# Optimization experiments

Hardware: AMD Instinct MI355X
Metric: run time of the kernel (lower is better)

## Reference

```python
import jax, jax.numpy as jnp
import numpy as np

H = 512   # hidden_state_sizes
E = 512   # embedding_size
L = 2     # num_rnn_layers
VGG = 4096


def gru_cell(x, h, Wu, bu, Wr, br, Wc, bc):
    # stacked = cat(x, h) along features; rows of W: first input, then hidden
    s = jnp.concatenate([x, h], axis=1)
    r = jax.nn.sigmoid(s @ Wr + br)
    u = jax.nn.sigmoid(s @ Wu + bu)
    s1 = jnp.concatenate([x, r * h], axis=1)
    c = jnp.tanh(s1 @ Wc + bc)
    return u * h + (1.0 - u) * c


def setup_inputs() -> dict:
    key = jax.random.key(0)
    ks = jax.random.split(key, 10)
    B, T, V = 128, 40, 10000
    N = E + H  # concat width (layer0: E+H == H+H since E==H)
    sc = float(np.sqrt(1.0 / N))
    return dict(
        xTokens=jax.random.randint(ks[0], (B, T), 0, V),
        vgg_fc7=jax.random.normal(ks[1], (B, VGG), jnp.float32),
        embedding=jax.random.normal(ks[2], (V, E), jnp.float32) * 0.02,
        W_in=jax.random.normal(ks[3], (VGG, H), jnp.float32) * float(np.sqrt(1.0 / VGG)),
        b_in=jnp.zeros((H,), jnp.float32),
        W_u=jax.random.normal(ks[4], (L, N, H), jnp.float32) * sc,
        b_u=jnp.zeros((L, H), jnp.float32),
        W_r=jax.random.normal(ks[5], (L, N, H), jnp.float32) * sc,
        b_r=jnp.zeros((L, H), jnp.float32),
        W_c=jax.random.normal(ks[6], (L, N, H), jnp.float32) * sc,
        b_c=jnp.zeros((L, H), jnp.float32),
        W_out=jax.random.normal(ks[7], (H, V), jnp.float32) * float(np.sqrt(1.0 / H)),
        b_out=jnp.zeros((V,), jnp.float32),
    )


def reference(xTokens, vgg_fc7, embedding, W_in, b_in, W_u, b_u, W_r, b_r,
              W_c, b_c, W_out, b_out):
    # initial hidden state from image features, shared across rnn layers
    h0 = jnp.tanh(vgg_fc7 @ W_in + b_in)                # [B,H]
    h = jnp.broadcast_to(h0, (L,) + h0.shape)           # [L,B,H]
    x = embedding[xTokens]                              # [B,T,E]
    xs = jnp.swapaxes(x, 0, 1)                          # [T,B,E] (scan over time)

    def step(h, xt):
        hs = []
        inp = xt
        for j in range(L):  # small fixed layer loop
            hj = gru_cell(inp, h[j], W_u[j], b_u[j], W_r[j], b_r[j], W_c[j], b_c[j])
            hs.append(hj)
            inp = hj
        logit = inp @ W_out + b_out                     # [B,V]
        return jnp.stack(hs), logit

    h_final, logits = jax.lax.scan(step, h, xs)         # logits [T,B,V]
    return jnp.swapaxes(logits, 0, 1), h_final
```

## Files before the change

### kernel.cpp

```cpp
#include <hip/hip_runtime.h>
#include <hip/hip_bf16.h>
#include <math.h>

typedef __bf16 bf16_t;
typedef __bf16 bf16x8 __attribute__((ext_vector_type(8)));
typedef float  f32x4 __attribute__((ext_vector_type(4)));
typedef float  f4    __attribute__((ext_vector_type(4)));
typedef float  f2    __attribute__((ext_vector_type(2)));
typedef unsigned short u16x4 __attribute__((ext_vector_type(4)));
typedef unsigned long long u64;

#define HS  512
#define BB  128
#define TT  40
#define VV  10000
#define VGGN 4096
#define SLOT ((size_t)65536)
#define NBLK 96
#define NGRID 256

#define CL(h, idx) ((((h) * 164) + (idx)) * 64)
#define CRH0(h,s) CL(h, (s))
#define CHB0(h,s) CL(h, 41 + (s))
#define CRH1(h,s) CL(h, 82 + (s))
#define CHB1(h,s) CL(h, 123 + (s))
#define XGR(t)    ((328 + (t)) * 64)
#define NSYNCW (368 * 64)

__device__ __forceinline__ void cst64(void* p, u64 v) {
  __hip_atomic_store((u64*)p, v, __ATOMIC_RELAXED, __HIP_MEMORY_SCOPE_AGENT);
}
__device__ __forceinline__ void cst32(float* p, float v) {
  __hip_atomic_store(p, v, __ATOMIC_RELAXED, __HIP_MEMORY_SCOPE_AGENT);
}

__device__ __forceinline__ void slot_inc(unsigned* sync, int line)
{
  __syncthreads();
  asm volatile("" ::: "memory");
  if (threadIdx.x == 0)
    __hip_atomic_fetch_add(&sync[line], 1u, __ATOMIC_RELAXED,
                           __HIP_MEMORY_SCOPE_AGENT);
}

template<int SLP>
__device__ __forceinline__ void slot_wait(unsigned* sync, int line,
                                          unsigned target)
{
  if (threadIdx.x == 0) {
    while (__hip_atomic_load(&sync[line], __ATOMIC_RELAXED,
                             __HIP_MEMORY_SCOPE_AGENT) < target)
      __builtin_amdgcn_s_sleep(SLP);
  }
  asm volatile("" ::: "memory");
  __syncthreads();
}

template<int SLP>
__device__ __forceinline__ void slot_wait2(unsigned* sync, int lineA,
                                           unsigned tA, int lineB, unsigned tB)
{
  if (threadIdx.x == 0) {
    while (__hip_atomic_load(&sync[lineA], __ATOMIC_RELAXED,
                             __HIP_MEMORY_SCOPE_AGENT) < tA)
      __builtin_amdgcn_s_sleep(SLP);
    while (__hip_atomic_load(&sync[lineB], __ATOMIC_RELAXED,
                             __HIP_MEMORY_SCOPE_AGENT) < tB)
      __builtin_amdgcn_s_sleep(SLP);
  }
  asm volatile("" ::: "memory");
  __syncthreads();
}

struct MiscArgs {
  unsigned* sync;
  const float *bu, *br, *bc;
  float* xbias;
  const float* vgg; bf16_t* vggb;
  const int* tok; const float* emb; bf16_t* Aemb;
};
__global__ __launch_bounds__(256) void prep_misc(MiscArgs M)
{
  const int b = blockIdx.x, tid = threadIdx.x;
  if (b == 0) {
    for (int i = tid; i < NSYNCW; i += 256) M.sync[i] = 0u;
  } else if (b < 13) {
    int i = (b - 1) * 256 + tid;
    if (i < 2 * 1536) {
      int j = i / 1536, qq = i % 1536;
      int g = qq >> 9, n = qq & 511;
      const float* src = (g == 0) ? M.bu : (g == 1) ? M.br : M.bc;
      M.xbias[i] = src[j * 512 + n];
    }
  } else if (b < 525) {
    int i = (b - 13) * 256 + tid;
    f4 v = ((const f4*)M.vgg)[i];
    M.vggb[i * 4 + 0] = (bf16_t)v[0]; M.vggb[i * 4 + 1] = (bf16_t)v[1];
    M.vggb[i * 4 + 2] = (bf16_t)v[2]; M.vggb[i * 4 + 3] = (bf16_t)v[3];
  } else {
    int blk = b - 525;
    int m = blk * 2 + (tid >> 7);
    int t = m >> 7, bb = m & 127;
    int tk = M.tok[bb * TT + t];
    int i = tid & 127;
    f4 v = *(const f4*)(M.emb + (size_t)tk * 512 + i * 4);
    bf16_t* dst = M.Aemb + (size_t)m * 512 + i * 4;
    dst[0] = (bf16_t)v[0]; dst[1] = (bf16_t)v[1];
    dst[2] = (bf16_t)v[2]; dst[3] = (bf16_t)v[3];
  }
}

struct PArgs {
  const bf16_t *Btru0, *Bt1ru, *Btc0, *Btc1;
  const float  *bu, *br, *bc, *hs0init;
  float *xg0;
  const bf16_t *Aemb, *Btx0;
  const float  *xbias;
  bf16_t *hb0_seq, *hb1_seq, *rh0s, *rh1s;
  const bf16_t *Wto;
  const float  *bo;
  float *out, *out_hfin;
  unsigned *sync;
};

template<int K, int NF>
__device__ __forceinline__ void tile_gemm64(
    const bf16_t* __restrict__ A0, const bf16_t* __restrict__ A1,
    const bf16_t* Bs, int wave, int lane, f32x4 (&acc)[NF])
{
  const int l15 = lane & 15, kg = lane >> 4;
  const int mw = wave * 16;
#pragma unroll
  for (int f = 0; f < NF; ++f)
#pragma unroll
    for (int e = 0; e < 4; ++e) acc[f][e] = 0.f;

#pragma unroll
  for (int kk = 0; kk < K; kk += 32) {
    const bf16_t* Asrc = (kk < 512) ? A0 : A1;
    const int kc = (kk < 512 ? kk : kk - 512) + kg * 8;
    bf16x8 a = *(const bf16x8*)(Asrc + (size_t)(mw + l15) * 512 + kc);
    bf16x8 b[NF];
#pragma unroll
    for (int f = 0; f < NF; ++f) {
      int row = f * 16 + l15;
      int byteoff = row * (2 * K) + ((2 * kk + 16 * kg) ^ ((row & 7) << 4));
      b[f] = *(const bf16x8*)((const char*)Bs + byteoff);
    }
#pragma unroll
    for (int f = 0; f < NF; ++f)
      acc[f] = __builtin_amdgcn_mfma_f32_16x16x32_bf16(a, b[f], acc[f], 0, 0, 0);
  }
}

template<int C>
__device__ __forceinline__ void publish64(
    bf16_t* dst, int row0, int n0, float (&v)[2][4],
    unsigned short (*tb)[36], int wave, int lane, int tid)
{
  const int l15 = lane & 15, kg = lane >> 4;
  const int mw = wave * 16;
  constexpr int NFp = C / 16;
#pragma unroll
  for (int f = 0; f < NFp; ++f)
#pragma unroll
    for (int e = 0; e < 4; ++e)
      tb[mw + kg * 4 + e][f * 16 + l15] =
          __builtin_bit_cast(unsigned short, (bf16_t)v[f][e]);
  __syncthreads();
  constexpr int NU = 64 * C / 4;
  constexpr int IT = (NU + 255) / 256;
#pragma unroll
  for (int it = 0; it < IT; ++it) {
    int lin = it * 256 + tid;
    if (lin < NU) {
      int row = lin / (C / 4);
      int cc  = (lin % (C / 4)) * 4;
      u16x4 pk = { tb[row][cc], tb[row][cc + 1], tb[row][cc + 2], tb[row][cc + 3] };
      cst64(dst + (size_t)(row0 + row) * 512 + n0 + cc, __builtin_bit_cast(u64, pk));
    }
  }
}

__global__ __launch_bounds__(256) void gru_persist(PArgs P)
{
  const int bid = blockIdx.x, tid = threadIdx.x;
  const int wave = tid >> 6, lane = tid & 63;
  const int l15 = lane & 15, kg = lane >> 4;
  unsigned* sync = P.sync;

  __threadfence();
  __syncthreads();

  if (bid >= NBLK) {
    const int w = bid - NBLK;
    const int wm = (wave >> 1) * 64, wn = (wave & 1) * 64;

    for (int tau = w; tau < TT * 12; tau += (NGRID - NBLK)) {
      const int t = tau / 12, nb = tau % 12;
      const int bm = t * 128, bn = nb * 128;
      const bf16_t* Ap = P.Aemb + (size_t)(bm + wm + l15) * 512 + kg * 8;
      const bf16_t* Bp = P.Btx0 + (size_t)(bn + wn + l15) * 512 + kg * 8;
      f32x4 acc[4][4];
#pragma unroll
      for (int i = 0; i < 4; ++i)
#pragma unroll
        for (int j = 0; j < 4; ++j)
#pragma unroll
          for (int e = 0; e < 4; ++e) acc[i][j][e] = 0.f;
      for (int kk = 0; kk < 512; kk += 32) {
        bf16x8 a[4], b[4];
#pragma unroll
        for (int i = 0; i < 4; ++i) a[i] = *(const bf16x8*)(Ap + (size_t)i * 16 * 512 + kk);
#pragma unroll
        for (int j = 0; j < 4; ++j) b[j] = *(const bf16x8*)(Bp + (size_t)j * 16 * 512 + kk);
#pragma unroll
        for (int i = 0; i < 4; ++i)
#pragma unroll
          for (int j = 0; j < 4; ++j)
            acc[i][j] = __builtin_amdgcn_mfma_f32_16x16x32_bf16(a[i], b[j], acc[i][j], 0, 0, 0);
      }
#pragma unroll
      for (int fm = 0; fm < 4; ++fm) {
#pragma unroll
        for (int fn = 0; fn < 4; ++fn) {
          int n = bn + wn + fn * 16 + l15;
          float bv = P.xbias[n];
#pragma unroll
          for (int e = 0; e < 4; ++e) {
            int m = bm + wm + fm * 16 + kg * 4 + e;
            cst32(&P.xg0[(size_t)m * 1536 + n], acc[fm][fn][e] + bv);
          }
        }
      }
      slot_inc(sync, XGR(t));
    }

    for (int tau = w; tau < TT * 79; tau += (NGRID - NBLK)) {
      const int t = tau / 79, nb = tau % 79;
      slot_wait2<64>(sync, CHB1(0, t + 1), 32u, CHB1(1, t + 1), 32u);
      const bf16_t* A = P.hb1_seq + (size_t)(t + 1) * SLOT;
      const bf16_t* Bp = P.Wto + (size_t)(nb * 128 + wn + l15) * 512 + kg * 8;
      f32x4 acc[4][4];
#pragma unroll
      for (int i = 0; i < 4; ++i)
#pragma unroll
        for (int j = 0; j < 4; ++j)
#pragma unroll
          for (int e = 0; e < 4; ++e) acc[i][j][e] = 0.f;
      for (int kk = 0; kk < 512; kk += 32) {
        bf16x8 a[4], b[4];
#pragma unroll
        for (int i = 0; i < 4; ++i)
          a[i] = *(const bf16x8*)(A + (size_t)(wm + i * 16 + l15) * 512 + kk + kg * 8);
#pragma unroll
        for (int j = 0; j < 4; ++j)
          b[j] = *(const bf16x8*)(Bp + (size_t)j * 16 * 512 + kk);
#pragma unroll
        for (int i = 0; i < 4; ++i)
#pragma unroll
          for (int j = 0; j < 4; ++j)
            acc[i][j] = __builtin_amdgcn_mfma_f32_16x16x32_bf16(a[i], b[j], acc[i][j], 0, 0, 0);
      }
#pragma unroll
      for (int fm = 0; fm < 4; ++fm) {
#pragma unroll
        for (int fn = 0; fn < 4; ++fn) {
          int n = nb * 128 + wn + fn * 16 + l15;
          if (n >= VV) continue;
          float bv = P.bo[n];
#pragma unroll
          for (int e = 0; e < 4; ++e) {
            int b_row = wm + fm * 16 + kg * 4 + e;
            P.out[(size_t)(b_row * TT + t) * VV + n] = acc[fm][fn][e] + bv;
          }
        }
      }
      __syncthreads();
    }
    return;
  }

  const int half = bid / 48;
  const int b2   = bid % 48;
  const int row0 = half * 64;
  const bool L0 = (b2 < 16);
  const int q  = L0 ? b2 : b2 - 16;
  const int n0 = L0 ? q * 32 : q * 16;
  const int mw = wave * 16;

  __shared__ bf16_t Bs[49152];
  __shared__ unsigned short tb[64][36];
  bf16_t* BsRU = Bs;
  bf16_t* BsC  = Bs + 32768;

  if (L0) {
    for (int c = tid; c < 4096; c += 256) {
      int row = c >> 6, cb = (c & 63) * 16;
      const bf16_t* src = (row < 32) ? P.Btru0 + (size_t)(n0 + row) * 512
                                     : P.Btru0 + (size_t)(512 + n0 + row - 32) * 512;
      *(f4*)((char*)BsRU + row * 1024 + (cb ^ ((row & 7) << 4))) =
          *(const f4*)((const char*)src + cb);
    }
    for (int c = tid; c < 2048; c += 256) {
      int row = c >> 6, cb = (c & 63) * 16;
      const bf16_t* src = P.Btc0 + (size_t)(n0 + row) * 512;
      *(f4*)((char*)BsC + row * 1024 + (cb ^ ((row & 7) << 4))) =
          *(const f4*)((const char*)src + cb);
    }
  } else {
    for (int c = tid; c < 4096; c += 256) {
      int row = c >> 7, cb = (c & 127) * 16;
      const bf16_t* src = (row < 16) ? P.Bt1ru + (size_t)(n0 + row) * 1024
                                     : P.Bt1ru + (size_t)(512 + n0 + row - 16) * 1024;
      *(f4*)((char*)BsRU + row * 2048 + (cb ^ ((row & 7) << 4))) =
          *(const f4*)((const char*)src + cb);
    }
    for (int c = tid; c < 2048; c += 256) {
      int row = c >> 7, cb = (c & 127) * 16;
      const bf16_t* src = P.Btc1 + (size_t)(n0 + row) * 1024;
      *(f4*)((char*)BsC + row * 2048 + (cb ^ ((row & 7) << 4))) =
          *(const f4*)((const char*)src + cb);
    }
  }
  __syncthreads();

  const int NFh = L0 ? 2 : 1;
  float hreg[2][4], ureg[2][4], rhv[2][4];
#pragma unroll
  for (int f = 0; f < 2; ++f)
#pragma unroll
    for (int e = 0; e < 4; ++e) {
      int row = row0 + mw + kg * 4 + e;
      hreg[f][e] = (f < NFh)
          ? P.hs0init[(size_t)row * 512 + n0 + f * 16 + l15] : 0.f;
      ureg[f][e] = 0.f; rhv[f][e] = 0.f;
    }

  if (L0) {
    for (int s = 0; s < 40; ++s) {
      slot_wait<8>(sync, XGR(s), 12u);
      const float* xg = P.xg0 + (size_t)s * 128 * 1536;
      float xvu[2][4], xvr[2][4];
#pragma unroll
      for (int f = 0; f < 2; ++f)
#pragma unroll
        for (int e = 0; e < 4; ++e) {
          int row = row0 + mw + kg * 4 + e;
          int col = n0 + f * 16 + l15;
          xvu[f][e] = xg[(size_t)row * 1536 + col];
          xvr[f][e] = xg[(size_t)row * 1536 + 512 + col];
        }
      if (s >= 1) slot_wait<8>(sync, CHB0(half, s), 16u);
      f32x4 acc4[4];
      const bf16_t* A0 = P.hb0_seq + (size_t)s * SLOT + (size_t)row0 * 512;
      tile_gemm64<512, 4>(A0, A0, BsRU, wave, lane, acc4);
#pragma unroll
      for (int f = 0; f < 2; ++f)
#pragma unroll
        for (int e = 0; e < 4; ++e) {
          float pu = acc4[f][e]     + xvu[f][e];
          float pr = acc4[f + 2][e] + xvr[f][e];
          ureg[f][e] = 1.f / (1.f + expf(-pu));
          rhv[f][e]  = (1.f / (1.f + expf(-pr))) * hreg[f][e];
        }
      publish64<32>(P.rh0s + (size_t)s * SLOT, row0, n0, rhv, tb, wave, lane, tid);
      slot_inc(sync, CRH0(half, s));
      float xvc[2][4];
#pragma unroll
      for (int f = 0; f < 2; ++f)
#pragma unroll
        for (int e = 0; e < 4; ++e) {
          int row = row0 + mw + kg * 4 + e;
          int col = n0 + f * 16 + l15;
          xvc[f][e] = xg[(size_t)row * 1536 + 1024 + col];
        }
      slot_wait<8>(sync, CRH0(half, s), 16u);

      f32x4 acc2[2];
      const bf16_t* Arh = P.rh0s + (size_t)s * SLOT + (size_t)row0 * 512;
      tile_gemm64<512, 2>(Arh, Arh, BsC, wave, lane, acc2);
#pragma unroll
      for (int f = 0; f < 2; ++f)
#pragma unroll
        for (int e = 0; e < 4; ++e) {
          float c = tanhf(acc2[f][e] + xvc[f][e]);
          float u = ureg[f][e];
          hreg[f][e] = u * hreg[f][e] + (1.f - u) * c;
          rhv[f][e] = hreg[f][e];
        }
      publish64<32>(P.hb0_seq + (size_t)(s + 1) * SLOT, row0, n0, rhv, tb, wave, lane, tid);
      slot_inc(sync, CHB0(half, s + 1));
    }
  } else {
    const float bvu = P.bu[512 + n0 + l15];
    const float bvr = P.br[512 + n0 + l15];
    const float bvc = P.bc[512 + n0 + l15];
    for (int s = 1; s <= 40; ++s) {
      if (s >= 2) slot_wait2<8>(sync, CHB0(half, s), 16u, CHB1(half, s - 1), 32u);
      else        slot_wait<8>(sync, CHB0(half, 1), 16u);
      f32x4 acc2[2];
      tile_gemm64<1024, 2>(P.hb0_seq + (size_t)s * SLOT + (size_t)row0 * 512,
                           P.hb1_seq + (size_t)(s - 1) * SLOT + (size_t)row0 * 512,
                           BsRU, wave, lane, acc2);
#pragma unroll
      for (int e = 0; e < 4; ++e) {
        float pu = acc2[0][e] + bvu;
        float pr = acc2[1][e] + bvr;
        ureg[0][e] = 1.f / (1.f + expf(-pu));
        rhv[0][e]  = (1.f / (1.f + expf(-pr))) * hreg[0][e];
      }
      publish64<16>(P.rh1s + (size_t)s * SLOT, row0, n0, rhv, tb, wave, lane, tid);
      slot_inc(sync, CRH1(half, s));
      slot_wait<8>(sync, CRH1(half, s), 32u);

      f32x4 acc1[1];
      tile_gemm64<1024, 1>(P.hb0_seq + (size_t)s * SLOT + (size_t)row0 * 512,
                           P.rh1s + (size_t)s * SLOT + (size_t)row0 * 512,
                           BsC, wave, lane, acc1);
#pragma unroll
      for (int e = 0; e < 4; ++e) {
        float c = tanhf(acc1[0][e] + bvc);
        float u = ureg[0][e];
        hreg[0][e] = u * hreg[0][e] + (1.f - u) * c;
        rhv[0][e] = hreg[0][e];
      }
      publish64<16>(P.hb1_seq + (size_t)s * SLOT, row0, n0, rhv, tb, wave, lane, tid);
      slot_inc(sync, CHB1(half, s));
    }
  }

  float* dst = P.out_hfin + (L0 ? 0 : 65536);
#pragma unroll
  for (int f = 0; f < 2; ++f)
    if (f < NFh)
#pragma unroll
      for (int e = 0; e < 4; ++e) {
        int row = row0 + mw + kg * 4 + e;
        dst[(size_t)row * 512 + n0 + f * 16 + l15] = hreg[f][e];
      }
}

__global__ __launch_bounds__(256) void h0_gemm(
    const bf16_t* __restrict__ vggb, const bf16_t* __restrict__ Wint,
    float* __restrict__ part)
{
  const int bn = blockIdx.x * 128, z = blockIdx.y, k0 = z * 512;
  const int tid = threadIdx.x;
  const int wave = tid >> 6, lane = tid & 63;
  const int wm = (wave >> 1) * 64, wn = (wave & 1) * 64;
  const int l15 = lane & 15, kg = lane >> 4;
  const bf16_t* Ap = vggb + (size_t)(wm + l15) * 4096 + k0 + kg * 8;
  const bf16_t* Bp = Wint + (size_t)(bn + wn + l15) * 4096 + k0 + kg * 8;
  f32x4 acc[4][4];
#pragma unroll
  for (int i = 0; i < 4; ++i)
#pragma unroll
    for (int j = 0; j < 4; ++j)
#pragma unroll
      for (int e = 0; e < 4; ++e) acc[i][j][e] = 0.f;
  for (int kk = 0; kk < 512; kk += 32) {
    bf16x8 a[4], b[4];
#pragma unroll
    for (int i = 0; i < 4; ++i) a[i] = *(const bf16x8*)(Ap + (size_t)i * 16 * 4096 + kk);
#pragma unroll
    for (int j = 0; j < 4; ++j) b[j] = *(const bf16x8*)(Bp + (size_t)j * 16 * 4096 + kk);
#pragma unroll
    for (int i = 0; i < 4; ++i)
#pragma unroll
      for (int j = 0; j < 4; ++j)
        acc[i][j] = __builtin_amdgcn_mfma_f32_16x16x32_bf16(a[i], b[j], acc[i][j], 0, 0, 0);
  }
#pragma unroll
  for (int fm = 0; fm < 4; ++fm)
#pragma unroll
    for (int fn = 0; fn < 4; ++fn) {
      int n = bn + wn + fn * 16 + l15;
#pragma unroll
      for (int e = 0; e < 4; ++e) {
        int m = wm + fm * 16 + kg * 4 + e;
        part[(size_t)z * SLOT + m * 512 + n] = acc[fm][fn][e];
      }
    }
}

__global__ void h0_fin(const float* __restrict__ part, const float* __restrict__ bin,
                       float* __restrict__ hs0init,
                       bf16_t* __restrict__ hb00, bf16_t* __restrict__ hb10)
{
  int i = blockIdx.x * 256 + threadIdx.x;
  int n = i & 511;
  float s = bin[n];
#pragma unroll
  for (int z = 0; z < 8; ++z) s += part[(size_t)z * SLOT + i];
  float v = tanhf(s);
  hs0init[i] = v;
  hb00[i] = (bf16_t)v; hb10[i] = (bf16_t)v;
}

struct TJob { const float* src; bf16_t* dst; int K; int dstld; };
struct TJobs4 { TJob j[4]; };
__global__ void transpose_gen(TJobs4 jobs)
{
  TJob jb = jobs.j[blockIdx.z];
  int k0 = blockIdx.x * 32;
  if (k0 >= jb.K) return;
  int n0 = blockIdx.y * 32;
  __shared__ float tile[32][33];
  int tx = threadIdx.x, ty = threadIdx.y;
#pragma unroll
  for (int r = 0; r < 4; ++r)
    tile[ty + 8 * r][tx] = jb.src[(size_t)(k0 + ty + 8 * r) * 512 + n0 + tx];
  __syncthreads();
#pragma unroll
  for (int r = 0; r < 4; ++r)
    jb.dst[(size_t)(n0 + ty + 8 * r) * jb.dstld + k0 + tx] = (bf16_t)tile[tx][ty + 8 * r];
}

struct TJobs6 { TJob j[6]; };
__global__ void transpose_gen6(TJobs6 jobs)
{
  TJob jb = jobs.j[blockIdx.z];
  int k0 = blockIdx.x * 32;
  if (k0 >= jb.K) return;
  int n0 = blockIdx.y * 32;
  __shared__ float tile[32][33];
  int tx = threadIdx.x, ty = threadIdx.y;
#pragma unroll
  for (int r = 0; r < 4; ++r)
    tile[ty + 8 * r][tx] = jb.src[(size_t)(k0 + ty + 8 * r) * 512 + n0 + tx];
  __syncthreads();
#pragma unroll
  for (int r = 0; r < 4; ++r)
    jb.dst[(size_t)(n0 + ty + 8 * r) * jb.dstld + k0 + tx] = (bf16_t)tile[tx][ty + 8 * r];
}

__global__ void transpose_wout(const float* __restrict__ W, bf16_t* __restrict__ dst)
{
  __shared__ float tile[32][33];
  int k0 = blockIdx.x * 32, n0 = blockIdx.y * 32;
  int tx = threadIdx.x, ty = threadIdx.y;
#pragma unroll
  for (int r = 0; r < 4; ++r) {
    int n = n0 + tx;
    tile[ty + 8 * r][tx] = (n < VV) ? W[(size_t)(k0 + ty + 8 * r) * VV + n] : 0.f;
  }
  __syncthreads();
#pragma unroll
  for (int r = 0; r < 4; ++r)
    dst[(size_t)(n0 + ty + 8 * r) * 512 + k0 + tx] = (bf16_t)tile[tx][ty + 8 * r];
}

extern "C" void kernel_launch(void* const* d_in, const int* in_sizes, int n_in,
                              void* d_out, int out_size, void* d_ws, size_t ws_size,
                              hipStream_t stream)
{
  const int*   tok = (const int*)  d_in[0];
  const float* vgg = (const float*)d_in[1];
  const float* emb = (const float*)d_in[2];
  const float* Win = (const float*)d_in[3];
  const float* bin = (const float*)d_in[4];
  const float* Wu  = (const float*)d_in[5];
  const float* bu  = (const float*)d_in[6];
  const float* Wr  = (const float*)d_in[7];
  const float* br  = (const float*)d_in[8];
  const float* Wc  = (const float*)d_in[9];
  const float* bc  = (const float*)d_in[10];
  const float* Wo  = (const float*)d_in[11];
  const float* bo  = (const float*)d_in[12];
  float* out = (float*)d_out;

  size_t off = 0;
  auto alloc = [&](size_t bytes) -> void* {
    void* p = (char*)d_ws + off;
    off += (bytes + 255) & ~(size_t)255;
    return p;
  };
  float*  hs0init = (float*) alloc(SLOT * 4);
  bf16_t* rh0s  = (bf16_t*)alloc(41 * SLOT * 2);
  bf16_t* rh1s  = (bf16_t*)alloc(41 * SLOT * 2);
  bf16_t* hb0_seq = (bf16_t*)alloc(41 * SLOT * 2);
  bf16_t* hb1_seq = (bf16_t*)alloc(41 * SLOT * 2);
  bf16_t* Aemb  = (bf16_t*)alloc((size_t)TT * BB * 512 * 2);
  float*  xg0   = (float*) alloc((size_t)TT * BB * 1536 * 4);
  bf16_t* Btx0  = (bf16_t*)alloc((size_t)1536 * 512 * 2);
  bf16_t* Btru0 = (bf16_t*)alloc((size_t)1024 * 512 * 2);
  bf16_t* Btc0  = (bf16_t*)alloc((size_t)512 * 512 * 2);
  bf16_t* Bt1ru = (bf16_t*)alloc((size_t)1024 * 1024 * 2);
  bf16_t* Btc1  = (bf16_t*)alloc((size_t)512 * 1024 * 2);
  bf16_t* Wto   = (bf16_t*)alloc((size_t)10112 * 512 * 2);
  bf16_t* Wint  = (bf16_t*)alloc((size_t)512 * 4096 * 2);
  bf16_t* vggb  = (bf16_t*)alloc((size_t)128 * 4096 * 2);
  float*  h0part= (float*) alloc(8 * SLOT * 4);
  float*  xbias = (float*) alloc(2 * 1536 * 4);
  unsigned* syncws = (unsigned*) alloc(NSYNCW * 4);
  if (off > ws_size) return;

  MiscArgs ma;
  ma.sync = syncws; ma.bu = bu; ma.br = br; ma.bc = bc; ma.xbias = xbias;
  ma.vgg = vgg; ma.vggb = vggb; ma.tok = tok; ma.emb = emb; ma.Aemb = Aemb;
  prep_misc<<<3085, 256, 0, stream>>>(ma);

  TJobs4 t4;
  t4.j[0] = { Wu,          Btx0,           512, 512 };
  t4.j[1] = { Wr,          Btx0 + 262144,  512, 512 };
  t4.j[2] = { Wc,          Btx0 + 524288,  512, 512 };
  t4.j[3] = { Win,         Wint,           4096, 4096 };
  transpose_gen<<<dim3(128, 16, 4), dim3(32, 8), 0, stream>>>(t4);
  TJobs6 t6;
  t6.j[0] = { Wu + 262144, Btru0,            512, 512 };
  t6.j[1] = { Wr + 262144, Btru0 + 262144,   512, 512 };
  t6.j[2] = { Wc + 262144, Btc0,             512, 512 };
  t6.j[3] = { Wu + 524288, Bt1ru,            1024, 1024 };
  t6.j[4] = { Wr + 524288, Bt1ru + 524288,   1024, 1024 };
  t6.j[5] = { Wc + 524288, Btc1,             1024, 1024 };
  transpose_gen6<<<dim3(32, 16, 6), dim3(32, 8), 0, stream>>>(t6);
  transpose_wout<<<dim3(16, 316), dim3(32, 8), 0, stream>>>(Wo, Wto);

  h0_gemm<<<dim3(4, 8), 256, 0, stream>>>(vggb, Wint, h0part);
  h0_fin<<<256, 256, 0, stream>>>(h0part, bin, hs0init, hb0_seq, hb1_seq);

  PArgs pa;
  pa.Btru0 = Btru0; pa.Bt1ru = Bt1ru; pa.Btc0 = Btc0; pa.Btc1 = Btc1;
  pa.bu = bu; pa.br = br; pa.bc = bc; pa.hs0init = hs0init;
  pa.xg0 = xg0; pa.Aemb = Aemb; pa.Btx0 = Btx0; pa.xbias = xbias;
  pa.hb0_seq = hb0_seq; pa.hb1_seq = hb1_seq;
  pa.rh0s = rh0s; pa.rh1s = rh1s;
  pa.Wto = Wto; pa.bo = bo; pa.out = out;
  pa.out_hfin = out + (size_t)BB * TT * VV;
  pa.sync = syncws;
  gru_persist<<<NGRID, 256, 0, stream>>>(pa);
}
```

Baseline: 579.0 us.

## Split layer-1 GEMMs by input half to start before previous hidden arrives

In the layer-1 GRU blocks, the gate GEMMs are split into the part that multiplies the layer-0 output and the part that multiplies the recurrent state. The layer-0 input contributions for both the reset/update and candidate gates are computed as soon as layer-0's output is ready, and only then does the block wait for the previous layer-1 step. This shortens the dependency-critical path inside the recurrent pipeline by overlapping work with the wait. The cost is a few more live accumulators.

```diff
diff --git a/kernel.cpp b/kernel.cpp
--- a/kernel.cpp
+++ b/kernel.cpp
@@ -153,6 +153,35 @@
   }
 }
 
+template<int NF, bool ACC>
+__device__ __forceinline__ void tile_gemm64_h(
+    const bf16_t* __restrict__ A, const bf16_t* Bs, int koff,
+    int wave, int lane, f32x4 (&acc)[NF])
+{
+  const int l15 = lane & 15, kg = lane >> 4;
+  const int mw = wave * 16;
+  if (!ACC) {
+#pragma unroll
+    for (int f = 0; f < NF; ++f)
+#pragma unroll
+      for (int e = 0; e < 4; ++e) acc[f][e] = 0.f;
+  }
+#pragma unroll
+  for (int kk = 0; kk < 512; kk += 32) {
+    bf16x8 a = *(const bf16x8*)(A + (size_t)(mw + l15) * 512 + kk + kg * 8);
+    bf16x8 b[NF];
+#pragma unroll
+    for (int f = 0; f < NF; ++f) {
+      int row = f * 16 + l15;
+      int byteoff = row * 2048 + ((2 * (koff + kk) + 16 * kg) ^ ((row & 7) << 4));
+      b[f] = *(const bf16x8*)((const char*)Bs + byteoff);
+    }
+#pragma unroll
+    for (int f = 0; f < NF; ++f)
+      acc[f] = __builtin_amdgcn_mfma_f32_16x16x32_bf16(a, b[f], acc[f], 0, 0, 0);
+  }
+}
+
 template<int C>
 __device__ __forceinline__ void publish64(
     bf16_t* dst, int row0, int n0, float (&v)[2][4],
@@ -397,30 +426,29 @@
     const float bvr = P.br[512 + n0 + l15];
     const float bvc = P.bc[512 + n0 + l15];
     for (int s = 1; s <= 40; ++s) {
-      if (s >= 2) slot_wait2<8>(sync, CHB0(half, s), 16u, CHB1(half, s - 1), 32u);
-      else        slot_wait<8>(sync, CHB0(half, 1), 16u);
-      f32x4 acc2[2];
-      tile_gemm64<1024, 2>(P.hb0_seq + (size_t)s * SLOT + (size_t)row0 * 512,
-                           P.hb1_seq + (size_t)(s - 1) * SLOT + (size_t)row0 * 512,
-                           BsRU, wave, lane, acc2);
+      slot_wait<8>(sync, CHB0(half, s), 16u);
+      const bf16_t* Ah0 = P.hb0_seq + (size_t)s * SLOT + (size_t)row0 * 512;
+      f32x4 accRU[2], accC[1];
+      tile_gemm64_h<2, false>(Ah0, BsRU, 0, wave, lane, accRU);
+      tile_gemm64_h<1, false>(Ah0, BsC,  0, wave, lane, accC);
+      if (s >= 2) slot_wait<8>(sync, CHB1(half, s - 1), 32u);
+      tile_gemm64_h<2, true>(P.hb1_seq + (size_t)(s - 1) * SLOT + (size_t)row0 * 512,
+                             BsRU, 512, wave, lane, accRU);
 #pragma unroll
       for (int e = 0; e < 4; ++e) {
-        float pu = acc2[0][e] + bvu;
-        float pr = acc2[1][e] + bvr;
+        float pu = accRU[0][e] + bvu;
+        float pr = accRU[1][e] + bvr;
         ureg[0][e] = 1.f / (1.f + expf(-pu));
         rhv[0][e]  = (1.f / (1.f + expf(-pr))) * hreg[0][e];
       }
       publish64<16>(P.rh1s + (size_t)s * SLOT, row0, n0, rhv, tb, wave, lane, tid);
       slot_inc(sync, CRH1(half, s));
       slot_wait<8>(sync, CRH1(half, s), 32u);
-
-      f32x4 acc1[1];
-      tile_gemm64<1024, 1>(P.hb0_seq + (size_t)s * SLOT + (size_t)row0 * 512,
-                           P.rh1s + (size_t)s * SLOT + (size_t)row0 * 512,
-                           BsC, wave, lane, acc1);
+      tile_gemm64_h<1, true>(P.rh1s + (size_t)s * SLOT + (size_t)row0 * 512,
+                             BsC, 512, wave, lane, accC);
 #pragma unroll
       for (int e = 0; e < 4; ++e) {
-        float c = tanhf(acc1[0][e] + bvc);
+        float c = tanhf(accC[0][e] + bvc);
         float u = ureg[0][e];
         hreg[0][e] = u * hreg[0][e] + (1.f - u) * c;
         rhv[0][e] = hreg[0][e];
```

New measurement: 532.6 us. -8.0%, faster.
